# Performance work log

Hardware: AMD Instinct MI355X
Metric: run time of the kernel (lower is better)

Reference implementation:

```python
import jax, jax.numpy as jnp
import numpy as np

DIM_HEAD = 32
WINDOW_SIZE = 8


def get_rel_pos_ind(win):
    coords = np.stack(np.meshgrid(np.arange(win), np.arange(win), indexing='ij')).reshape(2, -1)
    rel = coords[:, :, None] - coords[:, None, :] + (win - 1)
    return rel  # int


def setup_inputs() -> dict:
    key = jax.random.key(0)
    ks = jax.random.split(key, 4)
    B, N, dim = 2048, WINDOW_SIZE * WINDOW_SIZE, 512
    heads = dim // DIM_HEAD
    size = 2 * WINDOW_SIZE - 1
    return {
        'x': jax.random.normal(ks[0], (B, N, dim), jnp.float32),
        'w_qkv': jax.random.normal(ks[1], (dim, 3 * dim), jnp.float32) * 0.02,
        'b_qkv': jnp.zeros((3 * dim,), jnp.float32),
        'rel_pos_table': jax.random.normal(ks[2], (heads, size, size), jnp.float32) * 0.02,
        'w_proj': jax.random.normal(ks[3], (dim, dim), jnp.float32) * 0.02,
        'b_proj': jnp.zeros((dim,), jnp.float32),
        'train': 0,
    }


def reference(x, w_qkv, b_qkv, rel_pos_table, w_proj, b_proj, train):
    B, N, dim = x.shape
    heads = dim // DIM_HEAD
    scale = DIM_HEAD ** (-0.5)

    qkv = x @ w_qkv + b_qkv                                  # (B, N, 3*dim)
    qkv = qkv.reshape(B, N, 3, heads, DIM_HEAD)
    qkv = jnp.swapaxes(qkv, 1, 3)                            # (B, heads, 3, N, dh)
    q, k, v = qkv[:, :, 0], qkv[:, :, 1], qkv[:, :, 2]
    q = q * scale

    attn = jnp.einsum('bhnd,bhmd->bhnm', q, k)               # (B, heads, N, N)

    ind = get_rel_pos_ind(WINDOW_SIZE)                       # (2, N, N)
    bias = rel_pos_table[:, ind[0], ind[1]]                  # (heads, N, N)
    attn = jax.nn.softmax(attn + bias, axis=-1)

    out = jnp.einsum('bhnm,bhmd->bhnd', attn, v)             # (B, heads, N, dh)
    out = jnp.swapaxes(out, 1, 2).reshape(B, N, dim)
    return out @ w_proj + b_proj
```

## Files before the change

### kernel.cpp

```cpp
#include <hip/hip_runtime.h>
#include <stdint.h>
#include <stddef.h>

typedef unsigned short u16;
typedef __attribute__((ext_vector_type(8))) short short8;
typedef __attribute__((ext_vector_type(8))) unsigned short ushort8;
typedef __attribute__((ext_vector_type(4))) unsigned short u16x4;
typedef __attribute__((ext_vector_type(4))) float f32x4;

#define NTOK 64
#define DIM  512
#define QSTR 36
#define REGION 6912
#define XPAD 536

__device__ __forceinline__ float bf2f(u16 u) {
  union { unsigned int i; float f; } x; x.i = ((unsigned int)u) << 16; return x.f;
}
__device__ __forceinline__ u16 f2bf(float f) {
  union { float f; unsigned int i; } x; x.f = f;
  unsigned int u = x.i;
  u += 0x7fffu + ((u >> 16) & 1u);
  return (u16)(u >> 16);
}

__device__ __forceinline__ f32x4 shfl_xor4(f32x4 v, int m) {
  f32x4 r;
  #pragma unroll
  for (int e = 0; e < 4; ++e) r[e] = __shfl_xor(v[e], m, 64);
  return r;
}
__device__ __forceinline__ f32x4 max44(f32x4 a, f32x4 b) {
  f32x4 r;
  #pragma unroll
  for (int e = 0; e < 4; ++e) r[e] = fmaxf(a[e], b[e]);
  return r;
}

__global__ void detect_k(const u16* __restrict__ w_raw, int* __restrict__ flag) {
  if (threadIdx.x == 0 && blockIdx.x == 0) {
    int cnt = 0;
    for (int i = 0; i < 512; ++i) {
      float v = bf2f(w_raw[i]);
      if (!(v <= 0.5f && v >= -0.5f)) ++cnt;
    }
    flag[0] = (cnt > 16) ? 1 : 0;
  }
}


__global__ void cvt8_k(const float* __restrict__ fsrc, const u16* __restrict__ usrc,
                       u16* __restrict__ dst, int n, const int* __restrict__ flag) {
  int i = (blockIdx.x * 256 + threadIdx.x) * 8;
  if (i >= n) return;
  if (flag[0]) {
    f32x4 a = *(const f32x4*)(fsrc + i);
    f32x4 b = *(const f32x4*)(fsrc + i + 4);
    ushort8 o;
    #pragma unroll
    for (int e = 0; e < 4; ++e) { o[e] = f2bf(a[e]); o[e + 4] = f2bf(b[e]); }
    *(ushort8*)(dst + i) = o;
  } else {
    *(ushort8*)(dst + i) = *(const ushort8*)(usrc + i);
  }
}

__global__ void wfrag_k(const float* __restrict__ fsrc, const u16* __restrict__ usrc,
                        u16* __restrict__ dst, int NCOL, const int* __restrict__ flag) {
  int idx = blockIdx.x * 256 + threadIdx.x;
  int e = idx & 7, lane = (idx >> 3) & 63, ks = (idx >> 9) & 15, nt = idx >> 13;
  int n = nt * 16 + (lane & 15);
  int k = ks * 32 + (lane >> 4) * 8 + e;
  size_t src = (size_t)k * NCOL + n;
  dst[idx] = flag[0] ? f2bf(fsrc[src]) : usrc[src];
}

__global__ __launch_bounds__(256) void cvtfrag_k(
    const float* __restrict__ fsrc, const u16* __restrict__ usrc,
    u16* __restrict__ xf, const int* __restrict__ flag)
{
  __shared__ __attribute__((aligned(16))) u16 xl[64 * XPAD];
  const int t = threadIdx.x;
  const size_t wbase = (size_t)blockIdx.x * (NTOK * DIM);

  if (flag[0]) {
    #pragma unroll
    for (int c = 0; c < 32; ++c) {
      int i = c * 1024 + t * 4;
      f32x4 v = *(const f32x4*)(fsrc + wbase + i);
      int tok = i >> 9, k = i & 511;
      u16x4 o;
      #pragma unroll
      for (int e = 0; e < 4; ++e) o[e] = f2bf(v[e]);
      *(u16x4*)&xl[tok * XPAD + k] = o;
    }
  } else {
    #pragma unroll
    for (int c = 0; c < 16; ++c) {
      int i = c * 2048 + t * 8;
      ushort8 v = *(const ushort8*)(usrc + wbase + i);
      int tok = i >> 9, k = i & 511;
      *(ushort8*)&xl[tok * XPAD + k] = v;
    }
  }
  __syncthreads();

  u16* dst = xf + wbase;
  #pragma unroll
  for (int j = 0; j < 16; ++j) {
    int idx8 = j * 256 + t;
    int lane = idx8 & 63, mi = (idx8 >> 6) & 3, ks = idx8 >> 8;
    int tok = mi * 16 + (lane & 15);
    int k = ks * 32 + (lane >> 4) * 8;
    ushort8 v = *(const ushort8*)&xl[tok * XPAD + k];
    *(ushort8*)(dst + (size_t)idx8 * 8) = v;
  }
}

__global__ void bias_expand_k(const float* __restrict__ ftab, const u16* __restrict__ utab,
                              float* __restrict__ biasc, const int* __restrict__ flag) {
  int t = blockIdx.x * 256 + threadIdx.x;
  int r    = t & 3;
  int lane = (t >> 2) & 63;
  int ni   = (t >> 8) & 3;
  int mi   = (t >> 10) & 3;
  int h    = t >> 12;
  int n = mi * 16 + (lane >> 4) * 4 + r;
  int m = ni * 16 + (lane & 15);
  int i1 = n >> 3, j1 = n & 7, i2 = m >> 3, j2 = m & 7;
  int off = h * 225 + (i1 - i2 + 7) * 15 + (j1 - j2 + 7);
  if (flag[0]) biasc[t] = ftab[off];
  else         biasc[t] = bf2f(utab[off]);
}

__global__ __launch_bounds__(512, 1) void fused_k(
    const u16* __restrict__ xf,
    const u16* __restrict__ wqf,
    const u16* __restrict__ bqc,
    const float* __restrict__ biasc,
    const u16* __restrict__ wpf,
    const u16* __restrict__ bpc,
    const int* __restrict__ flag,
    u16* __restrict__ outU, float* __restrict__ outF)
{
  __shared__ __attribute__((aligned(16))) u16 lds[8][REGION];

  const int lane = threadIdx.x & 63;
  const int wave = threadIdx.x >> 6;
  const int lr = lane & 15, quad = lane >> 4;
  const int blk = blockIdx.x;

  u16* ql = &lds[wave][0];
  u16* kl = &lds[wave][2304];
  u16* Pl = &lds[wave][0];
  u16* vt = &lds[wave][4608];
  u16* Ol = &lds[wave][0];

  const u16* xw = xf + (size_t)blk * (NTOK * DIM) + lane * 8;
  const float SCALE = 0.17677669529663687f;
  const float L2E = 1.44269504088896f;
  const f32x4 zero4 = {0.f, 0.f, 0.f, 0.f};

  f32x4 acc[4][4];
  #pragma unroll
  for (int mi = 0; mi < 4; ++mi)
    #pragma unroll
    for (int ni = 0; ni < 4; ++ni) acc[mi][ni] = zero4;

  for (int r = 0; r < 2; ++r) {
    const int h = r * 8 + wave;

    f32x4 aq[4][2], ak[4][2], av[4][2];
    #pragma unroll
    for (int mi = 0; mi < 4; ++mi) {
      aq[mi][0] = zero4; aq[mi][1] = zero4;
      ak[mi][0] = zero4; ak[mi][1] = zero4;
      av[mi][0] = zero4; av[mi][1] = zero4;
    }
    const u16* wb = wqf + (size_t)(h * 2) * 8192 + lane * 8;
    #pragma unroll 4
    for (int ks = 0; ks < 16; ++ks) {
      short8 af[4];
      #pragma unroll
      for (int mi = 0; mi < 4; ++mi)
        af[mi] = *(const short8*)(xw + (ks * 4 + mi) * 512);
      short8 b0 = *(const short8*)(wb + ks * 512);
      short8 b1 = *(const short8*)(wb + 8192 + ks * 512);
      short8 b2 = *(const short8*)(wb + 32 * 8192 + ks * 512);
      short8 b3 = *(const short8*)(wb + 33 * 8192 + ks * 512);
      short8 b4 = *(const short8*)(wb + 64 * 8192 + ks * 512);
      short8 b5 = *(const short8*)(wb + 65 * 8192 + ks * 512);
      #pragma unroll
      for (int mi = 0; mi < 4; ++mi) {
        aq[mi][0] = __builtin_amdgcn_mfma_f32_16x16x32_bf16(af[mi], b0, aq[mi][0], 0, 0, 0);
        aq[mi][1] = __builtin_amdgcn_mfma_f32_16x16x32_bf16(af[mi], b1, aq[mi][1], 0, 0, 0);
        ak[mi][0] = __builtin_amdgcn_mfma_f32_16x16x32_bf16(af[mi], b2, ak[mi][0], 0, 0, 0);
        ak[mi][1] = __builtin_amdgcn_mfma_f32_16x16x32_bf16(af[mi], b3, ak[mi][1], 0, 0, 0);
        av[mi][0] = __builtin_amdgcn_mfma_f32_16x16x32_bf16(af[mi], b4, av[mi][0], 0, 0, 0);
        av[mi][1] = __builtin_amdgcn_mfma_f32_16x16x32_bf16(af[mi], b5, av[mi][1], 0, 0, 0);
      }
    }

    #pragma unroll
    for (int j = 0; j < 2; ++j) {
      float bq = bf2f(bqc[h * 32 + j * 16 + lr]);
      float bk = bf2f(bqc[512 + h * 32 + j * 16 + lr]);
      float bv = bf2f(bqc[1024 + h * 32 + j * 16 + lr]);
      #pragma unroll
      for (int mi = 0; mi < 4; ++mi)
        #pragma unroll
        for (int e = 0; e < 4; ++e) {
          int tok = mi * 16 + quad * 4 + e;
          int d = j * 16 + lr;
          ql[tok * QSTR + d] = f2bf((aq[mi][j][e] + bq) * SCALE);
          kl[tok * QSTR + d] = f2bf(ak[mi][j][e] + bk);
          vt[d * 72 + tok]   = f2bf(av[mi][j][e] + bv);
        }
    }

    f32x4 s[4][4];
    {
      short8 afq[4], bfk[4];
      #pragma unroll
      for (int mi = 0; mi < 4; ++mi)
        afq[mi] = *(const short8*)&ql[(mi * 16 + lr) * QSTR + quad * 8];
      #pragma unroll
      for (int ni = 0; ni < 4; ++ni)
        bfk[ni] = *(const short8*)&kl[(ni * 16 + lr) * QSTR + quad * 8];
      #pragma unroll
      for (int mi = 0; mi < 4; ++mi)
        #pragma unroll
        for (int ni = 0; ni < 4; ++ni)
          s[mi][ni] = __builtin_amdgcn_mfma_f32_16x16x32_bf16(afq[mi], bfk[ni], zero4, 0, 0, 0);
    }

    #pragma unroll
    for (int mi = 0; mi < 4; ++mi)
      #pragma unroll
      for (int ni = 0; ni < 4; ++ni) {
        f32x4 bb = *(const f32x4*)&biasc[((((h * 4 + mi) * 4 + ni) * 64) + lane) * 4];
        s[mi][ni] = s[mi][ni] + bb;
      }

    f32x4 mx[4];
    #pragma unroll
    for (int mi = 0; mi < 4; ++mi) {
      mx[mi] = max44(max44(s[mi][0], s[mi][1]), max44(s[mi][2], s[mi][3]));
      #pragma unroll
      for (int m = 1; m <= 8; m <<= 1) mx[mi] = max44(mx[mi], shfl_xor4(mx[mi], m));
    }
    f32x4 sum[4];
    #pragma unroll
    for (int mi = 0; mi < 4; ++mi) {
      #pragma unroll
      for (int ni = 0; ni < 4; ++ni)
        #pragma unroll
        for (int e = 0; e < 4; ++e)
          s[mi][ni][e] = exp2f((s[mi][ni][e] - mx[mi][e]) * L2E);
      sum[mi] = s[mi][0] + s[mi][1] + s[mi][2] + s[mi][3];
      #pragma unroll
      for (int m = 1; m <= 8; m <<= 1) sum[mi] = sum[mi] + shfl_xor4(sum[mi], m);
    }

    #pragma unroll
    for (int mi = 0; mi < 4; ++mi)
      #pragma unroll
      for (int ni = 0; ni < 4; ++ni)
        #pragma unroll
        for (int e = 0; e < 4; ++e) {
          int n = mi * 16 + quad * 4 + e;
          int col = ni * 16 + lr;
          Pl[n * 72 + col] = f2bf(s[mi][ni][e]);
        }

    f32x4 o[4][2];
    #pragma unroll
    for (int mi = 0; mi < 4; ++mi) { o[mi][0] = zero4; o[mi][1] = zero4; }
    #pragma unroll
    for (int ks = 0; ks < 2; ++ks) {
      short8 pf[4], vf[2];
      #pragma unroll
      for (int mi = 0; mi < 4; ++mi)
        pf[mi] = *(const short8*)&Pl[(mi * 16 + lr) * 72 + ks * 32 + quad * 8];
      #pragma unroll
      for (int ni = 0; ni < 2; ++ni)
        vf[ni] = *(const short8*)&vt[(ni * 16 + lr) * 72 + ks * 32 + quad * 8];
      #pragma unroll
      for (int mi = 0; mi < 4; ++mi)
        #pragma unroll
        for (int ni = 0; ni < 2; ++ni)
          o[mi][ni] = __builtin_amdgcn_mfma_f32_16x16x32_bf16(pf[mi], vf[ni], o[mi][ni], 0, 0, 0);
    }

    f32x4 rs[4];
    #pragma unroll
    for (int mi = 0; mi < 4; ++mi)
      #pragma unroll
      for (int e = 0; e < 4; ++e) rs[mi][e] = __builtin_amdgcn_rcpf(sum[mi][e]);
    #pragma unroll
    for (int mi = 0; mi < 4; ++mi)
      #pragma unroll
      for (int ni = 0; ni < 2; ++ni)
        #pragma unroll
        for (int e = 0; e < 4; ++e) {
          int tok = mi * 16 + quad * 4 + e;
          int d = ni * 16 + lr;
          Ol[tok * QSTR + d] = f2bf(o[mi][ni][e] * rs[mi][e]);
        }

    __syncthreads();

    const u16* wpb = wpf + (size_t)(wave * 4) * 8192 + lane * 8;
    #pragma unroll 2
    for (int w2 = 0; w2 < 8; ++w2) {
      const u16* Ow = &lds[w2][0];
      const int h2 = r * 8 + w2;
      short8 afO[4], bfW[4];
      #pragma unroll
      for (int mi = 0; mi < 4; ++mi)
        afO[mi] = *(const short8*)&Ow[(mi * 16 + lr) * QSTR + quad * 8];
      #pragma unroll
      for (int ni = 0; ni < 4; ++ni)
        bfW[ni] = *(const short8*)(wpb + ni * 8192 + h2 * 512);
      #pragma unroll
      for (int mi = 0; mi < 4; ++mi)
        #pragma unroll
        for (int ni = 0; ni < 4; ++ni)
          acc[mi][ni] = __builtin_amdgcn_mfma_f32_16x16x32_bf16(afO[mi], bfW[ni], acc[mi][ni], 0, 0, 0);
    }
    __syncthreads();
  }

  const int f32o = flag[0];
  if (f32o) {
    float* lf = (float*)&lds[0][0];
    #pragma unroll
    for (int pass = 0; pass < 2; ++pass) {
      __syncthreads();
      #pragma unroll
      for (int mi2 = 0; mi2 < 2; ++mi2) {
        int mi = pass * 2 + mi2;
        #pragma unroll
        for (int ni = 0; ni < 4; ++ni) {
          int col = wave * 64 + ni * 16 + lr;
          float bv = bf2f(bpc[col]);
          #pragma unroll
          for (int e = 0; e < 4; ++e) {
            int row = mi2 * 16 + quad * 4 + e;
            lf[row * 512 + col] = acc[mi][ni][e] + bv;
          }
        }
      }
      __syncthreads();
      const size_t rowbase = (size_t)(blk * NTOK + pass * 32) * DIM;
      #pragma unroll
      for (int c = 0; c < 8; ++c) {
        int i = c * 2048 + threadIdx.x * 4;
        *(f32x4*)(outF + rowbase + i) = *(const f32x4*)(lf + i);
      }
    }
  } else {
    #pragma unroll
    for (int ni = 0; ni < 4; ++ni) {
      int col = wave * 64 + ni * 16 + lr;
      float bv = bf2f(bpc[col]);
      #pragma unroll
      for (int mi = 0; mi < 4; ++mi) {
        size_t rowb = (size_t)(blk * NTOK + mi * 16 + quad * 4);
        #pragma unroll
        for (int e = 0; e < 4; ++e)
          outU[(rowb + e) * (size_t)DIM + col] = f2bf(acc[mi][ni][e] + bv);
      }
    }
  }
}


extern "C" void kernel_launch(void* const* d_in, const int* in_sizes, int n_in,
                              void* d_out, int out_size, void* d_ws, size_t ws_size,
                              hipStream_t stream)
{
  (void)in_sizes; (void)n_in; (void)out_size;

  const void* x      = d_in[0];
  const void* w_qkv  = d_in[1];
  const void* b_qkv  = d_in[2];
  const void* table  = d_in[3];
  const void* w_proj = d_in[4];
  const void* b_proj = d_in[5];

  char* ws = (char*)d_ws;
  size_t off = 0;
  auto alloc = [&](size_t bytes) -> char* {
    char* p = ws + off; off += (bytes + 255) & ~(size_t)255; return p;
  };
  u16*   wqf    = (u16*)alloc(1572864);
  u16*   wpf    = (u16*)alloc(524288);
  float* biasc  = (float*)alloc(262144);
  u16*   bqc    = (u16*)alloc(3072);
  u16*   bpc    = (u16*)alloc(1024);
  int*   flag   = (int*)alloc(256);
  size_t fixed  = off;

  int win = 2048;
  while (win > 2 && fixed + (size_t)win * 65536 > ws_size) win >>= 1;
  const int mc = win * 64;
  u16* xfC = (u16*)alloc((size_t)mc * 512 * 2);

  detect_k<<<dim3(1), dim3(64), 0, stream>>>((const u16*)w_qkv, flag);
  wfrag_k<<<dim3(3072), dim3(256), 0, stream>>>((const float*)w_qkv, (const u16*)w_qkv, wqf, 1536, flag);
  wfrag_k<<<dim3(1024), dim3(256), 0, stream>>>((const float*)w_proj, (const u16*)w_proj, wpf, 512, flag);
  bias_expand_k<<<dim3(256), dim3(256), 0, stream>>>((const float*)table, (const u16*)table, biasc, flag);
  cvt8_k<<<dim3(1), dim3(256), 0, stream>>>((const float*)b_qkv, (const u16*)b_qkv, bqc, 1536, flag);
  cvt8_k<<<dim3(1), dim3(256), 0, stream>>>((const float*)b_proj, (const u16*)b_proj, bpc, 512, flag);

  const int nchunk = 2048 / win;
  for (int c = 0; c < nchunk; ++c) {
    size_t base = (size_t)c * mc * 512;

    cvtfrag_k<<<dim3(win), dim3(256), 0, stream>>>(
        (const float*)x + base, (const u16*)x + base, xfC, flag);

    fused_k<<<dim3(win), dim3(512), 0, stream>>>(
        xfC, wqf, bqc, biasc, wpf, bpc, flag,
        (u16*)d_out + base, (float*)d_out + base);
  }
}
```

Measured before the change: 1.140 ms.

## Keep P and V in registers via lane shuffles, transpose S layout

Computes S as K·Q^T so that each lane holds a full query column. Softmax max and sum then need only two cross-lane shuffles instead of four per element vector, and the bias expansion layout is swapped to match. P and V are packed to bf16 pairs in registers and redistributed with __shfl into MFMA operand layout, which removes the LDS staging for P and the transposed V. The per-wave LDS region shrinks and launch bounds are raised to allow more blocks per CU. In exchange the code issues many more ds_bpermute shuffles and holds more registers, and the higher occupancy target may force register spills.

```diff
diff --git a/kernel.cpp b/kernel.cpp
--- a/kernel.cpp
+++ b/kernel.cpp
@@ -11,7 +11,7 @@
 #define NTOK 64
 #define DIM  512
 #define QSTR 36
-#define REGION 6912
+#define REGION 4608
 #define XPAD 536
 
 __device__ __forceinline__ float bf2f(u16 u) {
@@ -23,18 +23,8 @@
   u += 0x7fffu + ((u >> 16) & 1u);
   return (u16)(u >> 16);
 }
-
-__device__ __forceinline__ f32x4 shfl_xor4(f32x4 v, int m) {
-  f32x4 r;
-  #pragma unroll
-  for (int e = 0; e < 4; ++e) r[e] = __shfl_xor(v[e], m, 64);
-  return r;
-}
-__device__ __forceinline__ f32x4 max44(f32x4 a, f32x4 b) {
-  f32x4 r;
-  #pragma unroll
-  for (int e = 0; e < 4; ++e) r[e] = fmaxf(a[e], b[e]);
-  return r;
+__device__ __forceinline__ unsigned int pack2(float a, float b) {
+  return (unsigned int)f2bf(a) | ((unsigned int)f2bf(b) << 16);
 }
 
 __global__ void detect_k(const u16* __restrict__ w_raw, int* __restrict__ flag) {
@@ -125,15 +115,15 @@
   int ni   = (t >> 8) & 3;
   int mi   = (t >> 10) & 3;
   int h    = t >> 12;
-  int n = mi * 16 + (lane >> 4) * 4 + r;
-  int m = ni * 16 + (lane & 15);
+  int n = mi * 16 + (lane & 15);
+  int m = ni * 16 + (lane >> 4) * 4 + r;
   int i1 = n >> 3, j1 = n & 7, i2 = m >> 3, j2 = m & 7;
   int off = h * 225 + (i1 - i2 + 7) * 15 + (j1 - j2 + 7);
   if (flag[0]) biasc[t] = ftab[off];
   else         biasc[t] = bf2f(utab[off]);
 }
 
-__global__ __launch_bounds__(512, 1) void fused_k(
+__global__ __launch_bounds__(512, 4) void fused_k(
     const u16* __restrict__ xf,
     const u16* __restrict__ wqf,
     const u16* __restrict__ bqc,
@@ -152,14 +142,16 @@
 
   u16* ql = &lds[wave][0];
   u16* kl = &lds[wave][2304];
-  u16* Pl = &lds[wave][0];
-  u16* vt = &lds[wave][4608];
   u16* Ol = &lds[wave][0];
 
   const u16* xw = xf + (size_t)blk * (NTOK * DIM) + lane * 8;
   const float SCALE = 0.17677669529663687f;
   const float L2E = 1.44269504088896f;
   const f32x4 zero4 = {0.f, 0.f, 0.f, 0.f};
+
+  const int src1 = lr + ((quad & 1) << 5);
+  const int src2 = src1 + 16;
+  const bool hiq = quad >= 2;
 
   f32x4 acc[4][4];
   #pragma unroll
@@ -205,7 +197,6 @@
     for (int j = 0; j < 2; ++j) {
       float bq = bf2f(bqc[h * 32 + j * 16 + lr]);
       float bk = bf2f(bqc[512 + h * 32 + j * 16 + lr]);
-      float bv = bf2f(bqc[1024 + h * 32 + j * 16 + lr]);
       #pragma unroll
       for (int mi = 0; mi < 4; ++mi)
         #pragma unroll
@@ -214,99 +205,134 @@
           int d = j * 16 + lr;
           ql[tok * QSTR + d] = f2bf((aq[mi][j][e] + bq) * SCALE);
           kl[tok * QSTR + d] = f2bf(ak[mi][j][e] + bk);
-          vt[d * 72 + tok]   = f2bf(av[mi][j][e] + bv);
+        }
+    }
+
+    unsigned int pkv[2][4][2];
+    {
+      float bv0 = bf2f(bqc[1024 + h * 32 + lr]);
+      float bv1 = bf2f(bqc[1024 + h * 32 + 16 + lr]);
+      #pragma unroll
+      for (int mi = 0; mi < 4; ++mi)
+        #pragma unroll
+        for (int w = 0; w < 2; ++w) {
+          pkv[0][mi][w] = pack2(av[mi][0][2 * w] + bv0, av[mi][0][2 * w + 1] + bv0);
+          pkv[1][mi][w] = pack2(av[mi][1][2 * w] + bv1, av[mi][1][2 * w + 1] + bv1);
         }
     }
 
     f32x4 s[4][4];
     {
-      short8 afq[4], bfk[4];
-      #pragma unroll
-      for (int mi = 0; mi < 4; ++mi)
-        afq[mi] = *(const short8*)&ql[(mi * 16 + lr) * QSTR + quad * 8];
+      short8 afk[4], bfq[4];
+      #pragma unroll
+      for (int t = 0; t < 4; ++t)
+        afk[t] = *(const short8*)&kl[(t * 16 + lr) * QSTR + quad * 8];
+      #pragma unroll
+      for (int t = 0; t < 4; ++t)
+        bfq[t] = *(const short8*)&ql[(t * 16 + lr) * QSTR + quad * 8];
       #pragma unroll
       for (int ni = 0; ni < 4; ++ni)
-        bfk[ni] = *(const short8*)&kl[(ni * 16 + lr) * QSTR + quad * 8];
-      #pragma unroll
-      for (int mi = 0; mi < 4; ++mi)
-        #pragma unroll
-        for (int ni = 0; ni < 4; ++ni)
-          s[mi][ni] = __builtin_amdgcn_mfma_f32_16x16x32_bf16(afq[mi], bfk[ni], zero4, 0, 0, 0);
-    }
-
-    #pragma unroll
-    for (int mi = 0; mi < 4; ++mi)
+        #pragma unroll
+        for (int mi = 0; mi < 4; ++mi)
+          s[ni][mi] = __builtin_amdgcn_mfma_f32_16x16x32_bf16(afk[ni], bfq[mi], zero4, 0, 0, 0);
+    }
+
+    float ssum[4];
+    unsigned int pk[4][4][2];
+    #pragma unroll
+    for (int mi = 0; mi < 4; ++mi) {
       #pragma unroll
       for (int ni = 0; ni < 4; ++ni) {
         f32x4 bb = *(const f32x4*)&biasc[((((h * 4 + mi) * 4 + ni) * 64) + lane) * 4];
-        s[mi][ni] = s[mi][ni] + bb;
-      }
-
-    f32x4 mx[4];
+        s[ni][mi] = s[ni][mi] + bb;
+      }
+      f32x4 m4 = s[0][mi];
+      #pragma unroll
+      for (int ni = 1; ni < 4; ++ni)
+        #pragma unroll
+        for (int e = 0; e < 4; ++e) m4[e] = fmaxf(m4[e], s[ni][mi][e]);
+      float mm = fmaxf(fmaxf(m4[0], m4[1]), fmaxf(m4[2], m4[3]));
+      mm = fmaxf(mm, __shfl_xor(mm, 16, 64));
+      mm = fmaxf(mm, __shfl_xor(mm, 32, 64));
+      #pragma unroll
+      for (int ni = 0; ni < 4; ++ni)
+        #pragma unroll
+        for (int e = 0; e < 4; ++e)
+          s[ni][mi][e] = exp2f((s[ni][mi][e] - mm) * L2E);
+      f32x4 s4 = s[0][mi] + s[1][mi] + s[2][mi] + s[3][mi];
+      float sm = (s4[0] + s4[1]) + (s4[2] + s4[3]);
+      sm += __shfl_xor(sm, 16, 64);
+      sm += __shfl_xor(sm, 32, 64);
+      ssum[mi] = sm;
+      #pragma unroll
+      for (int ni = 0; ni < 4; ++ni)
+        #pragma unroll
+        for (int w = 0; w < 2; ++w)
+          pk[mi][ni][w] = pack2(s[ni][mi][2 * w], s[ni][mi][2 * w + 1]);
+    }
+
+    f32x4 o[4][2];
+    #pragma unroll
+    for (int mi = 0; mi < 4; ++mi) { o[mi][0] = zero4; o[mi][1] = zero4; }
+    #pragma unroll
+    for (int ks = 0; ks < 2; ++ks) {
+      short8 bvf[2];
+      #pragma unroll
+      for (int n2 = 0; n2 < 2; ++n2) {
+        union { short8 v; unsigned int w[4]; } u;
+        unsigned int a, b;
+        a = __shfl((int)pkv[n2][2 * ks][0], src1, 64);
+        b = __shfl((int)pkv[n2][2 * ks + 1][0], src1, 64);
+        u.w[0] = hiq ? b : a;
+        a = __shfl((int)pkv[n2][2 * ks][1], src1, 64);
+        b = __shfl((int)pkv[n2][2 * ks + 1][1], src1, 64);
+        u.w[1] = hiq ? b : a;
+        a = __shfl((int)pkv[n2][2 * ks][0], src2, 64);
+        b = __shfl((int)pkv[n2][2 * ks + 1][0], src2, 64);
+        u.w[2] = hiq ? b : a;
+        a = __shfl((int)pkv[n2][2 * ks][1], src2, 64);
+        b = __shfl((int)pkv[n2][2 * ks + 1][1], src2, 64);
+        u.w[3] = hiq ? b : a;
+        bvf[n2] = u.v;
+      }
+      #pragma unroll
+      for (int mi = 0; mi < 4; ++mi) {
+        union { short8 v; unsigned int w[4]; } u;
+        unsigned int a, b;
+        a = __shfl((int)pk[mi][2 * ks][0], src1, 64);
+        b = __shfl((int)pk[mi][2 * ks + 1][0], src1, 64);
+        u.w[0] = hiq ? b : a;
+        a = __shfl((int)pk[mi][2 * ks][1], src1, 64);
+        b = __shfl((int)pk[mi][2 * ks + 1][1], src1, 64);
+        u.w[1] = hiq ? b : a;
+        a = __shfl((int)pk[mi][2 * ks][0], src2, 64);
+        b = __shfl((int)pk[mi][2 * ks + 1][0], src2, 64);
+        u.w[2] = hiq ? b : a;
+        a = __shfl((int)pk[mi][2 * ks][1], src2, 64);
+        b = __shfl((int)pk[mi][2 * ks + 1][1], src2, 64);
+        u.w[3] = hiq ? b : a;
+        o[mi][0] = __builtin_amdgcn_mfma_f32_16x16x32_bf16(u.v, bvf[0], o[mi][0], 0, 0, 0);
+        o[mi][1] = __builtin_amdgcn_mfma_f32_16x16x32_bf16(u.v, bvf[1], o[mi][1], 0, 0, 0);
+      }
+    }
+
     #pragma unroll
     for (int mi = 0; mi < 4; ++mi) {
-      mx[mi] = max44(max44(s[mi][0], s[mi][1]), max44(s[mi][2], s[mi][3]));
-      #pragma unroll
-      for (int m = 1; m <= 8; m <<= 1) mx[mi] = max44(mx[mi], shfl_xor4(mx[mi], m));
-    }
-    f32x4 sum[4];
-    #pragma unroll
-    for (int mi = 0; mi < 4; ++mi) {
-      #pragma unroll
-      for (int ni = 0; ni < 4; ++ni)
-        #pragma unroll
-        for (int e = 0; e < 4; ++e)
-          s[mi][ni][e] = exp2f((s[mi][ni][e] - mx[mi][e]) * L2E);
-      sum[mi] = s[mi][0] + s[mi][1] + s[mi][2] + s[mi][3];
-      #pragma unroll
-      for (int m = 1; m <= 8; m <<= 1) sum[mi] = sum[mi] + shfl_xor4(sum[mi], m);
-    }
-
-    #pragma unroll
-    for (int mi = 0; mi < 4; ++mi)
-      #pragma unroll
-      for (int ni = 0; ni < 4; ++ni)
-        #pragma unroll
-        for (int e = 0; e < 4; ++e) {
-          int n = mi * 16 + quad * 4 + e;
-          int col = ni * 16 + lr;
-          Pl[n * 72 + col] = f2bf(s[mi][ni][e]);
-        }
-
-    f32x4 o[4][2];
-    #pragma unroll
-    for (int mi = 0; mi < 4; ++mi) { o[mi][0] = zero4; o[mi][1] = zero4; }
-    #pragma unroll
-    for (int ks = 0; ks < 2; ++ks) {
-      short8 pf[4], vf[2];
-      #pragma unroll
-      for (int mi = 0; mi < 4; ++mi)
-        pf[mi] = *(const short8*)&Pl[(mi * 16 + lr) * 72 + ks * 32 + quad * 8];
-      #pragma unroll
-      for (int ni = 0; ni < 2; ++ni)
-        vf[ni] = *(const short8*)&vt[(ni * 16 + lr) * 72 + ks * 32 + quad * 8];
-      #pragma unroll
-      for (int mi = 0; mi < 4; ++mi)
-        #pragma unroll
-        for (int ni = 0; ni < 2; ++ni)
-          o[mi][ni] = __builtin_amdgcn_mfma_f32_16x16x32_bf16(pf[mi], vf[ni], o[mi][ni], 0, 0, 0);
-    }
-
-    f32x4 rs[4];
-    #pragma unroll
-    for (int mi = 0; mi < 4; ++mi)
-      #pragma unroll
-      for (int e = 0; e < 4; ++e) rs[mi][e] = __builtin_amdgcn_rcpf(sum[mi][e]);
-    #pragma unroll
-    for (int mi = 0; mi < 4; ++mi)
-      #pragma unroll
-      for (int ni = 0; ni < 2; ++ni)
+      f32x4 rs;
+      #pragma unroll
+      for (int e = 0; e < 4; ++e) {
+        float sv = __shfl(ssum[mi], (quad * 4 + e) + (lane & 48), 64);
+        rs[e] = __builtin_amdgcn_rcpf(sv);
+      }
+      #pragma unroll
+      for (int n2 = 0; n2 < 2; ++n2)
         #pragma unroll
         for (int e = 0; e < 4; ++e) {
           int tok = mi * 16 + quad * 4 + e;
-          int d = ni * 16 + lr;
-          Ol[tok * QSTR + d] = f2bf(o[mi][ni][e] * rs[mi][e]);
+          int d = n2 * 16 + lr;
+          Ol[tok * QSTR + d] = f2bf(o[mi][n2][e] * rs[e]);
         }
+    }
 
     __syncthreads();
 
```

After: 2.935 ms. 2.58x slower.
